# Kernel tuning notes

Measured on AMD Instinct MI355X. Metric: run time of the kernel, lower is better.

Reference implementation:

```python
import jax, jax.numpy as jnp
import numpy as np

N, DIM = 4096, 1024

def setup_inputs() -> dict:
    key = jax.random.key(0)
    ks = jax.random.split(key, 5)
    scale = 1.0 / np.sqrt(DIM)
    return {
        "x": jax.random.normal(ks[0], (N, DIM), dtype=jnp.float32),
        "Wq": jax.random.normal(ks[1], (DIM, DIM), dtype=jnp.float32) * scale,
        "bq": jax.random.normal(ks[2], (DIM,), dtype=jnp.float32) * 0.01,
        "Wk": jax.random.normal(ks[3], (DIM, DIM), dtype=jnp.float32) * scale,
        "bk": jax.random.normal(ks[4], (DIM,), dtype=jnp.float32) * 0.01,
    }

def reference(x, Wq, bq, Wk, bk):
    # torch nn.Linear: y = x @ W.T + b
    q = x @ Wq.T + bq            # [N, D]
    k = x @ Wk.T + bk            # [N, D]
    scores = q @ k.T             # [N, N] (no 1/sqrt(d) scaling, as in source)
    attn = jax.nn.softmax(scores, axis=-1)
    return attn @ x              # weighted pooling over raw x (no value proj)
```

## Files before the change

kernel.cpp:

```cpp
#include <hip/hip_runtime.h>
#include <hip/hip_bf16.h>
#include <hip/hip_fp16.h>
#include <stdint.h>


using half8   = __attribute__((ext_vector_type(8))) _Float16;
using float4v = __attribute__((ext_vector_type(4))) float;
using int4v   = __attribute__((ext_vector_type(4))) int;
using uint2v  = __attribute__((ext_vector_type(2))) unsigned int;

#define QS        (6.0f / 32768.0f)
#define INV_S     (32768.0f / 6.0f)
#define INV_S256  (128.0f / 6.0f)
#define C_HH      (65536.0f * QS * QS)
#define C_X       (256.0f * QS * QS)

#define SX        (6.0f / 32768.0f)
#define SW        (0.25f / 32768.0f)
#define P_HH      (65536.0f * SX * SW)
#define P_X       (256.0f * SX * SW)

#define GLOAD_LDS16(gptr, ldsptr)                                              \
  __builtin_amdgcn_global_load_lds(                                            \
      (__attribute__((address_space(1))) void*)(uintptr_t)(gptr),              \
      (__attribute__((address_space(3))) void*)(unsigned)(uintptr_t)(ldsptr),  \
      16, 0, 0)

__device__ __forceinline__ void barrier_raw() {
  asm volatile("" ::: "memory");
  __builtin_amdgcn_s_barrier();
  asm volatile("" ::: "memory");
}

__device__ __forceinline__ int swz3(int row) {
  return (((row >> 2) & 3) << 1) ^ (row & 3);
}

__global__ __launch_bounds__(256, 2) void gemm_s_stats(
    const int8_t* __restrict__ Ahi, const int8_t* __restrict__ Alo,
    const int8_t* __restrict__ Bhi, const int8_t* __restrict__ Blo,
    _Float16* __restrict__ E, float2* __restrict__ stats)
{
  __shared__ __align__(16) int8_t smem[65536];
  int8_t* sAh = smem;
  int8_t* sAl = smem + 16384;
  int8_t* sBh = smem + 32768;
  int8_t* sBl = smem + 49152;

  const int tid  = threadIdx.x;
  const int wave = tid >> 6;
  const int lane = tid & 63;
  const int quad = lane >> 4;
  const int t16  = lane & 15;
  const int wm   = wave & 1;
  const int wn   = wave >> 1;

  const int L    = blockIdx.y * 32 + blockIdx.x;
  const int xcd  = L & 7;
  const int idx  = L >> 3;
  const int bx   = xcd * 4 + (idx & 3);
  const int by   = idx >> 2;
  const int row0 = by * 128;
  const int col0 = bx * 128;

  const int seg  = lane & 3;
  const int rsub = lane >> 2;
  const int segS = (seg - rsub) & 3;
  const int rch  = ((quad + t16) & 3) * 16;

  const int offA0 = (row0 + wave * 16 + rsub) * 2048 + segS * 16;
  const int offA1 = offA0 + 64 * 2048;
  const int offB0 = (col0 + wave * 16 + rsub) * 2048 + segS * 16;
  const int offB1 = offB0 + 64 * 2048;
  const int ldsT0 = (wave * 16) * 64;
  const int ldsT1 = (64 + wave * 16) * 64;

  int4v hh[4][4], cc[4][4];
#pragma unroll
  for (int i = 0; i < 4; ++i)
#pragma unroll
    for (int j = 0; j < 4; ++j) {
      hh[i][j] = (int4v){0, 0, 0, 0};
      cc[i][j] = (int4v){0, 0, 0, 0};
    }

  auto stage_AhBh = [&](int ks, int b) {
    const int k0 = ks * 64;
    GLOAD_LDS16(Ahi + offA0 + k0, sAh + b * 8192 + ldsT0);
    GLOAD_LDS16(Ahi + offA1 + k0, sAh + b * 8192 + ldsT1);
    GLOAD_LDS16(Bhi + offB0 + k0, sBh + b * 8192 + ldsT0);
    GLOAD_LDS16(Bhi + offB1 + k0, sBh + b * 8192 + ldsT1);
  };
  auto stage_Bl = [&](int ks, int b) {
    const int k0 = ks * 64;
    GLOAD_LDS16(Blo + offB0 + k0, sBl + b * 8192 + ldsT0);
    GLOAD_LDS16(Blo + offB1 + k0, sBl + b * 8192 + ldsT1);
  };
  auto stage_Al = [&](int ks, int b) {
    const int k0 = ks * 64;
    GLOAD_LDS16(Alo + offA0 + k0, sAl + b * 8192 + ldsT0);
    GLOAD_LDS16(Alo + offA1 + k0, sAl + b * 8192 + ldsT1);
  };

  stage_AhBh(0, 0);
  stage_Bl(0, 0);
  stage_Al(0, 0);

  int buf = 0;
  for (int ks = 0; ks < 16; ++ks) {
    asm volatile("s_waitcnt vmcnt(4)" ::: "memory");
    barrier_raw();
    if (ks < 15) stage_AhBh(ks + 1, buf ^ 1);

    int4v ah[4], bh[4];
#pragma unroll
    for (int i = 0; i < 4; ++i)
      ah[i] = *(const int4v*)(sAh + buf * 8192 +
                              (wm * 64 + i * 16 + t16) * 64 + rch);
#pragma unroll
    for (int j = 0; j < 4; ++j)
      bh[j] = *(const int4v*)(sBh + buf * 8192 +
                              (wn * 64 + j * 16 + t16) * 64 + rch);

    __builtin_amdgcn_s_setprio(1);
#pragma unroll
    for (int i = 0; i < 4; ++i)
#pragma unroll
      for (int j = 0; j < 4; ++j)
        hh[i][j] = __builtin_amdgcn_mfma_i32_16x16x64_i8(ah[i], bh[j], hh[i][j], 0, 0, 0);
    __builtin_amdgcn_s_setprio(0);

    if (ks < 15) asm volatile("s_waitcnt vmcnt(6)" ::: "memory");
    else         asm volatile("s_waitcnt vmcnt(2)" ::: "memory");
    barrier_raw();
    if (ks < 15) stage_Bl(ks + 1, buf ^ 1);

    int4v bl[4];
#pragma unroll
    for (int j = 0; j < 4; ++j)
      bl[j] = *(const int4v*)(sBl + buf * 8192 +
                              (wn * 64 + j * 16 + t16) * 64 + rch);

    __builtin_amdgcn_s_setprio(1);
#pragma unroll
    for (int i = 0; i < 4; ++i)
#pragma unroll
      for (int j = 0; j < 4; ++j)
        cc[i][j] = __builtin_amdgcn_mfma_i32_16x16x64_i8(ah[i], bl[j], cc[i][j], 0, 0, 0);
    __builtin_amdgcn_s_setprio(0);

    if (ks < 15) asm volatile("s_waitcnt vmcnt(6)" ::: "memory");
    else         asm volatile("s_waitcnt vmcnt(0)" ::: "memory");
    barrier_raw();
    if (ks < 15) stage_Al(ks + 1, buf ^ 1);

    int4v al[4];
#pragma unroll
    for (int i = 0; i < 4; ++i)
      al[i] = *(const int4v*)(sAl + buf * 8192 +
                              (wm * 64 + i * 16 + t16) * 64 + rch);

    __builtin_amdgcn_s_setprio(1);
#pragma unroll
    for (int i = 0; i < 4; ++i)
#pragma unroll
      for (int j = 0; j < 4; ++j)
        cc[i][j] = __builtin_amdgcn_mfma_i32_16x16x64_i8(al[i], bh[j], cc[i][j], 0, 0, 0);
    __builtin_amdgcn_s_setprio(0);

    buf ^= 1;
  }

  float* red = (float*)smem;

  float vv[4][4][4];
  float rmax[4][4];
#pragma unroll
  for (int i = 0; i < 4; ++i)
#pragma unroll
    for (int r = 0; r < 4; ++r) {
      float mx = -3.0e38f;
#pragma unroll
      for (int j = 0; j < 4; ++j) {
        float v = C_HH * (float)hh[i][j][r] + C_X * (float)cc[i][j][r];
        vv[i][j][r] = v;
        mx = fmaxf(mx, v);
      }
      mx = fmaxf(mx, __shfl_xor(mx, 1));
      mx = fmaxf(mx, __shfl_xor(mx, 2));
      mx = fmaxf(mx, __shfl_xor(mx, 4));
      mx = fmaxf(mx, __shfl_xor(mx, 8));
      rmax[i][r] = mx;
    }
  if (t16 == 0) {
#pragma unroll
    for (int i = 0; i < 4; ++i)
#pragma unroll
      for (int r = 0; r < 4; ++r)
        red[wn * 128 + wm * 64 + i * 16 + quad * 4 + r] = rmax[i][r];
  }
  __syncthreads();

  float mrow[4][4];
#pragma unroll
  for (int i = 0; i < 4; ++i)
#pragma unroll
    for (int r = 0; r < 4; ++r) {
      const int row = wm * 64 + i * 16 + quad * 4 + r;
      mrow[i][r] = fmaxf(red[row], red[128 + row]);
    }

  float rsum[4][4];
#pragma unroll
  for (int i = 0; i < 4; ++i)
#pragma unroll
    for (int r = 0; r < 4; ++r) {
      float s = 0.f;
#pragma unroll
      for (int j = 0; j < 4; ++j) {
        float e = __expf(vv[i][j][r] - mrow[i][r]);
        vv[i][j][r] = e;
        s += e;
      }
      s += __shfl_xor(s, 1);
      s += __shfl_xor(s, 2);
      s += __shfl_xor(s, 4);
      s += __shfl_xor(s, 8);
      rsum[i][r] = s;
    }
  if (t16 == 0) {
#pragma unroll
    for (int i = 0; i < 4; ++i)
#pragma unroll
      for (int r = 0; r < 4; ++r)
        red[256 + wn * 128 + wm * 64 + i * 16 + quad * 4 + r] = rsum[i][r];
  }

  uint16_t* img = (uint16_t*)(smem + 32768);
#pragma unroll
  for (int i = 0; i < 4; ++i)
#pragma unroll
    for (int j = 0; j < 4; ++j)
#pragma unroll
      for (int r = 0; r < 4; ++r) {
        const int row  = wm * 64 + i * 16 + quad * 4 + r;
        const int col  = wn * 64 + j * 16 + t16;
        const int colS = col ^ (((quad << 1) ^ r) << 3);
        _Float16 h = (_Float16)vv[i][j][r];
        img[row * 128 + colS] = *(const uint16_t*)&h;
      }
  __syncthreads();

#pragma unroll
  for (int it = 0; it < 8; ++it) {
    const int row    = wave * 32 + it * 4 + quad;
    const int chunkS = t16 ^ swz3(row);
    int4v v = *(const int4v*)&img[row * 128 + chunkS * 8];
    *(int4v*)&E[(size_t)(row0 + row) * 4096 + col0 + t16 * 8] = v;
  }

  if (wn == 0 && t16 == 0) {
#pragma unroll
    for (int i = 0; i < 4; ++i)
#pragma unroll
      for (int r = 0; r < 4; ++r) {
        const int row = wm * 64 + i * 16 + quad * 4 + r;
        const float l = red[256 + row] + red[256 + 128 + row];
        stats[(size_t)(row0 + row) * 32 + bx] =
            make_float2(mrow[i][r], l);
      }
  }
}

__global__ __launch_bounds__(256, 2) void gemm_proj_i8(
    const int8_t* __restrict__ Ahi, const int8_t* __restrict__ Alo,
    const int8_t* __restrict__ Bhi, const int8_t* __restrict__ Blo,
    const float* __restrict__ biasQ, const float* __restrict__ biasK,
    int8_t* __restrict__ Ch, int8_t* __restrict__ Cl)
{
  __shared__ __align__(16) int8_t smem[65536];
  int8_t* sAh = smem;
  int8_t* sAl = smem + 16384;
  int8_t* sBh = smem + 32768;
  int8_t* sBl = smem + 49152;

  const int tid  = threadIdx.x;
  const int wave = tid >> 6;
  const int lane = tid & 63;
  const int quad = lane >> 4;
  const int t16  = lane & 15;
  const int wm   = wave & 1;
  const int wn   = wave >> 1;

  const int L    = blockIdx.y * 16 + blockIdx.x;
  const int xcd  = L & 7;
  const int idx  = L >> 3;
  const int bx   = xcd * 2 + (idx & 1);
  const int by   = idx >> 1;
  const int row0 = by * 128;
  const int col0 = bx * 128;

  const int seg  = lane & 3;
  const int rsub = lane >> 2;
  const int segS = (seg - rsub) & 3;
  const int rch  = ((quad + t16) & 3) * 16;

  const int offA0 = (row0 + wave * 16 + rsub) * 1024 + segS * 16;
  const int offA1 = offA0 + 64 * 1024;
  const int offB0 = (col0 + wave * 16 + rsub) * 1024 + segS * 16;
  const int offB1 = offB0 + 64 * 1024;
  const int ldsT0 = (wave * 16) * 64;
  const int ldsT1 = (64 + wave * 16) * 64;

  int4v hh[4][4], cc[4][4];
#pragma unroll
  for (int i = 0; i < 4; ++i)
#pragma unroll
    for (int j = 0; j < 4; ++j) {
      hh[i][j] = (int4v){0, 0, 0, 0};
      cc[i][j] = (int4v){0, 0, 0, 0};
    }

  auto stage_AhBh = [&](int ks, int b) {
    const int k0 = ks * 64;
    GLOAD_LDS16(Ahi + offA0 + k0, sAh + b * 8192 + ldsT0);
    GLOAD_LDS16(Ahi + offA1 + k0, sAh + b * 8192 + ldsT1);
    GLOAD_LDS16(Bhi + offB0 + k0, sBh + b * 8192 + ldsT0);
    GLOAD_LDS16(Bhi + offB1 + k0, sBh + b * 8192 + ldsT1);
  };
  auto stage_Bl = [&](int ks, int b) {
    const int k0 = ks * 64;
    GLOAD_LDS16(Blo + offB0 + k0, sBl + b * 8192 + ldsT0);
    GLOAD_LDS16(Blo + offB1 + k0, sBl + b * 8192 + ldsT1);
  };
  auto stage_Al = [&](int ks, int b) {
    const int k0 = ks * 64;
    GLOAD_LDS16(Alo + offA0 + k0, sAl + b * 8192 + ldsT0);
    GLOAD_LDS16(Alo + offA1 + k0, sAl + b * 8192 + ldsT1);
  };

  stage_AhBh(0, 0);
  stage_Bl(0, 0);
  stage_Al(0, 0);

  int buf = 0;
  for (int ks = 0; ks < 16; ++ks) {
    asm volatile("s_waitcnt vmcnt(4)" ::: "memory");
    barrier_raw();
    if (ks < 15) stage_AhBh(ks + 1, buf ^ 1);

    int4v ah[4], bh[4];
#pragma unroll
    for (int i = 0; i < 4; ++i)
      ah[i] = *(const int4v*)(sAh + buf * 8192 +
                              (wm * 64 + i * 16 + t16) * 64 + rch);
#pragma unroll
    for (int j = 0; j < 4; ++j)
      bh[j] = *(const int4v*)(sBh + buf * 8192 +
                              (wn * 64 + j * 16 + t16) * 64 + rch);

    __builtin_amdgcn_s_setprio(1);
#pragma unroll
    for (int i = 0; i < 4; ++i)
#pragma unroll
      for (int j = 0; j < 4; ++j)
        hh[i][j] = __builtin_amdgcn_mfma_i32_16x16x64_i8(ah[i], bh[j], hh[i][j], 0, 0, 0);
    __builtin_amdgcn_s_setprio(0);

    if (ks < 15) asm volatile("s_waitcnt vmcnt(6)" ::: "memory");
    else         asm volatile("s_waitcnt vmcnt(2)" ::: "memory");
    barrier_raw();
    if (ks < 15) stage_Bl(ks + 1, buf ^ 1);

    int4v bl[4];
#pragma unroll
    for (int j = 0; j < 4; ++j)
      bl[j] = *(const int4v*)(sBl + buf * 8192 +
                              (wn * 64 + j * 16 + t16) * 64 + rch);

    __builtin_amdgcn_s_setprio(1);
#pragma unroll
    for (int i = 0; i < 4; ++i)
#pragma unroll
      for (int j = 0; j < 4; ++j)
        cc[i][j] = __builtin_amdgcn_mfma_i32_16x16x64_i8(ah[i], bl[j], cc[i][j], 0, 0, 0);
    __builtin_amdgcn_s_setprio(0);

    if (ks < 15) asm volatile("s_waitcnt vmcnt(6)" ::: "memory");
    else         asm volatile("s_waitcnt vmcnt(0)" ::: "memory");
    barrier_raw();
    if (ks < 15) stage_Al(ks + 1, buf ^ 1);

    int4v al[4];
#pragma unroll
    for (int i = 0; i < 4; ++i)
      al[i] = *(const int4v*)(sAl + buf * 8192 +
                              (wm * 64 + i * 16 + t16) * 64 + rch);

    __builtin_amdgcn_s_setprio(1);
#pragma unroll
    for (int i = 0; i < 4; ++i)
#pragma unroll
      for (int j = 0; j < 4; ++j)
        cc[i][j] = __builtin_amdgcn_mfma_i32_16x16x64_i8(al[i], bh[j], cc[i][j], 0, 0, 0);
    __builtin_amdgcn_s_setprio(0);

    buf ^= 1;
  }

  uint16_t* img = (uint16_t*)(smem + 32768);
#pragma unroll
  for (int i = 0; i < 4; ++i) {
#pragma unroll
    for (int j = 0; j < 4; ++j) {
      const int ccol = col0 + wn * 64 + j * 16 + t16;
      const float* bp = (ccol < 1024) ? biasQ : (biasK - 1024);
#pragma unroll
      for (int r = 0; r < 4; ++r) {
        float v = P_HH * (float)hh[i][j][r] + P_X * (float)cc[i][j][r] + bp[ccol];
        int hi = (int)lrintf(v * INV_S256);
        hi = hi > 127 ? 127 : (hi < -127 ? -127 : hi);
        int lo = (int)lrintf(v * INV_S - 256.0f * (float)hi);
        lo = lo > 127 ? 127 : (lo < -127 ? -127 : lo);
        const int row  = wm * 64 + i * 16 + quad * 4 + r;
        const int col  = wn * 64 + j * 16 + t16;
        const int colS = col ^ (((quad << 1) ^ r) << 3);
        img[row * 128 + colS] = (uint16_t)((hi & 0xff) | ((lo & 0xff) << 8));
      }
    }
  }
  __syncthreads();

#pragma unroll
  for (int it = 0; it < 8; ++it) {
    const int row    = wave * 32 + it * 4 + quad;
    const int chunkS = t16 ^ swz3(row);
    int4v p = *(const int4v*)&img[row * 128 + chunkS * 8];
    const unsigned w0 = (unsigned)p[0], w1 = (unsigned)p[1];
    const unsigned w2 = (unsigned)p[2], w3 = (unsigned)p[3];
    uint2v hw, lw;
    hw[0] = (w0 & 0xffu) | (((w0 >> 16) & 0xffu) << 8) |
            ((w1 & 0xffu) << 16) | (((w1 >> 16) & 0xffu) << 24);
    hw[1] = (w2 & 0xffu) | (((w2 >> 16) & 0xffu) << 8) |
            ((w3 & 0xffu) << 16) | (((w3 >> 16) & 0xffu) << 24);
    lw[0] = ((w0 >> 8) & 0xffu) | (((w0 >> 24) & 0xffu) << 8) |
            (((w1 >> 8) & 0xffu) << 16) | ((w1 >> 24) << 24);
    lw[1] = ((w2 >> 8) & 0xffu) | (((w2 >> 24) & 0xffu) << 8) |
            (((w3 >> 8) & 0xffu) << 16) | ((w3 >> 24) << 24);
    const size_t go = (size_t)(row0 + row) * 2048 + col0 + t16 * 8;
    *(uint2v*)&Ch[go] = hw;
    *(uint2v*)&Cl[go] = lw;
  }
}

__global__ __launch_bounds__(256, 2) void gemm_av(
    const uint16_t* __restrict__ E, const uint16_t* __restrict__ B,
    const float2* __restrict__ stats, float* __restrict__ out)
{
  __shared__ __align__(16) uint16_t stg[2][12288];
  __shared__ _Float16 betaS[128 * 33];

  const int L      = blockIdx.x;
  const int xcd    = L & 7;
  const int rest   = L >> 3;
  const int colb   = rest & 15;
  const int bandHi = rest >> 4;
  const int band   = xcd + 8 * bandHi;
  const int row0   = band * 128;
  const int col0   = colb * 64;

  const int tid  = threadIdx.x;
  const int wave = tid >> 6;
  const int lane = tid & 63;
  const int quad = lane >> 4;
  const int t16  = lane & 15;
  const int wm   = wave & 1;
  const int wn   = wave >> 1;

  const int r8   = lane >> 3;
  const int c8   = lane & 7;
  const int srcC = (c8 - r8) & 7;

  int offA[4], offBx[2];
#pragma unroll
  for (int p = 0; p < 4; ++p)
    offA[p] = (row0 + p * 32 + wave * 8 + r8) * 4096 + srcC * 8;
#pragma unroll
  for (int p = 0; p < 2; ++p)
    offBx[p] = (col0 + p * 32 + wave * 8 + r8) * 4096 + srcC * 8;

  auto stage_s = [&](int s, int b) {
    const int k0h = s * 64;
    uint16_t* sA = &stg[b][0];
    uint16_t* sB = &stg[b][8192];
#pragma unroll
    for (int p = 0; p < 4; ++p)
      GLOAD_LDS16(E + offA[p] + k0h, &sA[(p * 32 + wave * 8) * 64]);
#pragma unroll
    for (int p = 0; p < 2; ++p)
      GLOAD_LDS16(B + offBx[p] + k0h, &sB[(p * 32 + wave * 8) * 64]);
  };

  stage_s(0, 0);

  if (tid < 128) {
    const int row = row0 + tid;
    float2 st[32];
    float m = -3.0e38f;
#pragma unroll
    for (int t = 0; t < 32; ++t) {
      st[t] = stats[(size_t)row * 32 + t];
      m = fmaxf(m, st[t].x);
    }
    float l = 0.f;
#pragma unroll
    for (int t = 0; t < 32; ++t) l += st[t].y * __expf(st[t].x - m);
    const float inv = 1.0f / l;
#pragma unroll
    for (int t = 0; t < 32; ++t)
      betaS[tid * 33 + t] = (_Float16)(__expf(st[t].x - m) * inv);
  }
  asm volatile("s_waitcnt vmcnt(0)" ::: "memory");
  __syncthreads();

  float4v acc[4][2];
#pragma unroll
  for (int i = 0; i < 4; ++i)
#pragma unroll
    for (int j = 0; j < 2; ++j)
      acc[i][j] = (float4v){0.f, 0.f, 0.f, 0.f};

  int buf = 0;
  for (int s = 0; s < 64; ++s) {
    if (s < 63) stage_s(s + 1, buf ^ 1);

    const int t = s >> 1;
    _Float16 bb[4];
#pragma unroll
    for (int i = 0; i < 4; ++i)
      bb[i] = betaS[(wm * 64 + i * 16 + t16) * 33 + t];

    const uint16_t* sA = &stg[buf][0];
    const uint16_t* sB = &stg[buf][8192];

    half8 af[2][4], bf[2][2];
#pragma unroll
    for (int ks = 0; ks < 2; ++ks) {
#pragma unroll
      for (int i = 0; i < 4; ++i) {
        const int row = wm * 64 + i * 16 + t16;
        const int ch  = (ks * 4 + quad + (t16 & 7)) & 7;
        af[ks][i] = *(const half8*)&sA[row * 64 + ch * 8];
        half8 bs;
#pragma unroll
        for (int c = 0; c < 8; ++c) bs[c] = bb[i];
        af[ks][i] = af[ks][i] * bs;
      }
#pragma unroll
      for (int j = 0; j < 2; ++j) {
        const int row = wn * 32 + j * 16 + t16;
        const int ch  = (ks * 4 + quad + (t16 & 7)) & 7;
        bf[ks][j] = *(const half8*)&sB[row * 64 + ch * 8];
      }
    }

    __builtin_amdgcn_s_setprio(1);
#pragma unroll
    for (int ks = 0; ks < 2; ++ks)
#pragma unroll
      for (int i = 0; i < 4; ++i)
#pragma unroll
        for (int j = 0; j < 2; ++j)
          acc[i][j] = __builtin_amdgcn_mfma_f32_16x16x32_f16(af[ks][i], bf[ks][j], acc[i][j], 0, 0, 0);
    __builtin_amdgcn_s_setprio(0);

    if (s < 63) asm volatile("s_waitcnt vmcnt(0)" ::: "memory");
    barrier_raw();
    buf ^= 1;
  }

  float* img = (float*)stg;
#pragma unroll
  for (int i = 0; i < 4; ++i)
#pragma unroll
    for (int j = 0; j < 2; ++j)
#pragma unroll
      for (int r = 0; r < 4; ++r) {
        const int row  = wm * 64 + i * 16 + quad * 4 + r;
        const int col  = wn * 32 + j * 16 + t16;
        const int colS = col ^ (swz3(row) << 2);
        img[row * 64 + colS] = acc[i][j][r];
      }
  __syncthreads();

#pragma unroll
  for (int it = 0; it < 8; ++it) {
    const int row    = wave * 32 + it * 4 + quad;
    const int chunkS = t16 ^ swz3(row);
    float4v v = *(const float4v*)&img[row * 64 + chunkS * 4];
    *(float4v*)&out[(size_t)(row0 + row) * 1024 + col0 + t16 * 4] = v;
  }
}

__global__ __launch_bounds__(256) void quantT(
    const float* __restrict__ x, const float* __restrict__ Wq,
    const float* __restrict__ Wk,
    int8_t* __restrict__ xhi, int8_t* __restrict__ xlo,
    int8_t* __restrict__ whi, int8_t* __restrict__ wlo,
    uint16_t* __restrict__ xT)
{
  if (blockIdx.x < 6144) {
    int i = blockIdx.x * 256 + threadIdx.x;
    const float* src; int8_t* dh; int8_t* dl; int idx; float s256, s;
    if (i < 1048576)      { src = x;  idx = i;           dh = xhi; dl = xlo;
                            s256 = INV_S256; s = INV_S; }
    else if (i < 1310720) { src = Wq; idx = i - 1048576; dh = whi; dl = wlo;
                            s256 = 512.0f; s = 131072.0f; }
    else                  { src = Wk; idx = i - 1310720; dh = whi + 1048576;
                            dl = wlo + 1048576; s256 = 512.0f; s = 131072.0f; }
    float4 v = ((const float4*)src)[idx];
    float vv[4] = {v.x, v.y, v.z, v.w};
    int hp = 0, lp = 0;
#pragma unroll
    for (int c = 0; c < 4; ++c) {
      int h = (int)lrintf(vv[c] * s256);
      h = h > 127 ? 127 : (h < -127 ? -127 : h);
      int l = (int)lrintf(vv[c] * s - 256.0f * (float)h);
      l = l > 127 ? 127 : (l < -127 ? -127 : l);
      hp |= (h & 0xff) << (8 * c);
      lp |= (l & 0xff) << (8 * c);
    }
    ((int*)dh)[idx] = hp;
    ((int*)dl)[idx] = lp;
  } else {
    __shared__ float tile[32][33];
    const int tb = blockIdx.x - 6144;
    const int bx = tb & 31;
    const int by = tb >> 5;
    const int tx = threadIdx.x & 31;
    const int ty = threadIdx.x >> 5;
#pragma unroll
    for (int p = 0; p < 4; ++p) {
      const int row = by * 32 + ty + p * 8;
      tile[ty + p * 8][tx] = x[(size_t)row * 1024 + bx * 32 + tx];
    }
    __syncthreads();
#pragma unroll
    for (int p = 0; p < 4; ++p) {
      const int oc = ty + p * 8;
      __half hv = __float2half_rn(tile[tx][oc]);
      xT[(size_t)(bx * 32 + oc) * 4096 + by * 32 + tx] = *(uint16_t*)&hv;
    }
  }
}

extern "C" void kernel_launch(void* const* d_in, const int* in_sizes, int n_in,
                              void* d_out, int out_size, void* d_ws, size_t ws_size,
                              hipStream_t stream) {
  const int N = 4096, D = 1024;
  const float* x  = (const float*)d_in[0];
  const float* Wq = (const float*)d_in[1];
  const float* bq = (const float*)d_in[2];
  const float* Wk = (const float*)d_in[3];
  const float* bk = (const float*)d_in[4];
  float* out = (float*)d_out;

  char* w = (char*)d_ws;
  const size_t MiB = 1024 * 1024;
  int8_t*    xq_hi  = (int8_t*)   (w + 0  * MiB);
  int8_t*    xq_lo  = (int8_t*)   (w + 4  * MiB);
  int8_t*    Wqk_hi = (int8_t*)   (w + 8  * MiB);
  int8_t*    Wqk_lo = (int8_t*)   (w + 10 * MiB);
  int8_t*    qk_hi  = (int8_t*)   (w + 12 * MiB);
  int8_t*    qk_lo  = (int8_t*)   (w + 20 * MiB);
  _Float16*  E      = (_Float16*) (w + 36 * MiB);
  float2*    stats  = (float2*)   (w + 68 * MiB);
  uint16_t*  xTh    = (uint16_t*) (w + 72 * MiB);

  quantT<<<10240, 256, 0, stream>>>(x, Wq, Wk, xq_hi, xq_lo, Wqk_hi, Wqk_lo,
                                    xTh);

  gemm_proj_i8<<<dim3(2048 / 128, N / 128), 256, 0, stream>>>(
      xq_hi, xq_lo, Wqk_hi, Wqk_lo, bq, bk, qk_hi, qk_lo);

  gemm_s_stats<<<dim3(N / 128, N / 128), 256, 0, stream>>>(
      qk_hi, qk_lo, qk_hi + 1024, qk_lo + 1024, E, stats);

  gemm_av<<<512, 256, 0, stream>>>((const uint16_t*)E, xTh, stats, out);

  (void)in_sizes; (void)n_in; (void)out_size; (void)ws_size;
}
```

Baseline: 214.7 us.

## Fuse all stages into one persistent cooperative kernel with grid syncs

Wraps the quantize/transpose, projection GEMM, score-plus-stats GEMM and attention-times-x GEMM into device functions. It runs them all in a single cooperative kernel of 512 resident blocks, separated by grid-wide syncs, which removes three kernel launch boundaries and their tail gaps. The projection and score tile mappings lose the previous XCD-aware block remapping, which may hurt L2 locality. The fixed block count serializes the score tiles two per block. If the cooperative launch fails, it falls back to the original four separate launches.

```diff
diff --git a/kernel.cpp b/kernel.cpp
--- a/kernel.cpp
+++ b/kernel.cpp
@@ -1,7 +1,10 @@
 #include <hip/hip_runtime.h>
 #include <hip/hip_bf16.h>
 #include <hip/hip_fp16.h>
+#include <hip/hip_cooperative_groups.h>
 #include <stdint.h>
+
+namespace cg = cooperative_groups;
 
 
 using half8   = __attribute__((ext_vector_type(8))) _Float16;
@@ -36,267 +39,77 @@
   return (((row >> 2) & 3) << 1) ^ (row & 3);
 }
 
-__global__ __launch_bounds__(256, 2) void gemm_s_stats(
-    const int8_t* __restrict__ Ahi, const int8_t* __restrict__ Alo,
-    const int8_t* __restrict__ Bhi, const int8_t* __restrict__ Blo,
-    _Float16* __restrict__ E, float2* __restrict__ stats)
-{
-  __shared__ __align__(16) int8_t smem[65536];
+
+__device__ __forceinline__ void quant_unit(
+    int u, int tid, const float* x, const float* Wq, const float* Wk,
+    int8_t* xhi, int8_t* xlo, int8_t* whi, int8_t* wlo)
+{
+  int i = u * 256 + tid;
+  const float* src; int8_t* dh; int8_t* dl; int idx; float s256, s;
+  if (i < 1048576)      { src = x;  idx = i;           dh = xhi; dl = xlo;
+                          s256 = INV_S256; s = INV_S; }
+  else if (i < 1310720) { src = Wq; idx = i - 1048576; dh = whi; dl = wlo;
+                          s256 = 512.0f; s = 131072.0f; }
+  else                  { src = Wk; idx = i - 1310720; dh = whi + 1048576;
+                          dl = wlo + 1048576; s256 = 512.0f; s = 131072.0f; }
+  float4 v = ((const float4*)src)[idx];
+  float vv[4] = {v.x, v.y, v.z, v.w};
+  int hp = 0, lp = 0;
+#pragma unroll
+  for (int c = 0; c < 4; ++c) {
+    int h = (int)lrintf(vv[c] * s256);
+    h = h > 127 ? 127 : (h < -127 ? -127 : h);
+    int l = (int)lrintf(vv[c] * s - 256.0f * (float)h);
+    l = l > 127 ? 127 : (l < -127 ? -127 : l);
+    hp |= (h & 0xff) << (8 * c);
+    lp |= (l & 0xff) << (8 * c);
+  }
+  ((int*)dh)[idx] = hp;
+  ((int*)dl)[idx] = lp;
+}
+
+__device__ __forceinline__ void transpose_unit(
+    int u, int tid, int8_t* smem, const float* x, uint16_t* xT)
+{
+  float (*tile)[33] = (float(*)[33])smem;
+  const int tb = u - 6144;
+  const int bx = tb & 31;
+  const int by = tb >> 5;
+  const int tx = tid & 31;
+  const int ty = tid >> 5;
+#pragma unroll
+  for (int p = 0; p < 4; ++p) {
+    const int row = by * 32 + ty + p * 8;
+    tile[ty + p * 8][tx] = x[(size_t)row * 1024 + bx * 32 + tx];
+  }
+  __syncthreads();
+#pragma unroll
+  for (int p = 0; p < 4; ++p) {
+    const int oc = ty + p * 8;
+    __half hv = __float2half_rn(tile[tx][oc]);
+    xT[(size_t)(bx * 32 + oc) * 4096 + by * 32 + tx] = *(uint16_t*)&hv;
+  }
+  __syncthreads();
+}
+
+__device__ __forceinline__ void proj_tile(
+    int bx, int by, int tid, int8_t* smem,
+    const int8_t* Ahi, const int8_t* Alo,
+    const int8_t* Bhi, const int8_t* Blo,
+    const float* biasQ, const float* biasK,
+    int8_t* Ch, int8_t* Cl)
+{
   int8_t* sAh = smem;
   int8_t* sAl = smem + 16384;
   int8_t* sBh = smem + 32768;
   int8_t* sBl = smem + 49152;
 
-  const int tid  = threadIdx.x;
   const int wave = tid >> 6;
   const int lane = tid & 63;
   const int quad = lane >> 4;
   const int t16  = lane & 15;
   const int wm   = wave & 1;
   const int wn   = wave >> 1;
-
-  const int L    = blockIdx.y * 32 + blockIdx.x;
-  const int xcd  = L & 7;
-  const int idx  = L >> 3;
-  const int bx   = xcd * 4 + (idx & 3);
-  const int by   = idx >> 2;
-  const int row0 = by * 128;
-  const int col0 = bx * 128;
-
-  const int seg  = lane & 3;
-  const int rsub = lane >> 2;
-  const int segS = (seg - rsub) & 3;
-  const int rch  = ((quad + t16) & 3) * 16;
-
-  const int offA0 = (row0 + wave * 16 + rsub) * 2048 + segS * 16;
-  const int offA1 = offA0 + 64 * 2048;
-  const int offB0 = (col0 + wave * 16 + rsub) * 2048 + segS * 16;
-  const int offB1 = offB0 + 64 * 2048;
-  const int ldsT0 = (wave * 16) * 64;
-  const int ldsT1 = (64 + wave * 16) * 64;
-
-  int4v hh[4][4], cc[4][4];
-#pragma unroll
-  for (int i = 0; i < 4; ++i)
-#pragma unroll
-    for (int j = 0; j < 4; ++j) {
-      hh[i][j] = (int4v){0, 0, 0, 0};
-      cc[i][j] = (int4v){0, 0, 0, 0};
-    }
-
-  auto stage_AhBh = [&](int ks, int b) {
-    const int k0 = ks * 64;
-    GLOAD_LDS16(Ahi + offA0 + k0, sAh + b * 8192 + ldsT0);
-    GLOAD_LDS16(Ahi + offA1 + k0, sAh + b * 8192 + ldsT1);
-    GLOAD_LDS16(Bhi + offB0 + k0, sBh + b * 8192 + ldsT0);
-    GLOAD_LDS16(Bhi + offB1 + k0, sBh + b * 8192 + ldsT1);
-  };
-  auto stage_Bl = [&](int ks, int b) {
-    const int k0 = ks * 64;
-    GLOAD_LDS16(Blo + offB0 + k0, sBl + b * 8192 + ldsT0);
-    GLOAD_LDS16(Blo + offB1 + k0, sBl + b * 8192 + ldsT1);
-  };
-  auto stage_Al = [&](int ks, int b) {
-    const int k0 = ks * 64;
-    GLOAD_LDS16(Alo + offA0 + k0, sAl + b * 8192 + ldsT0);
-    GLOAD_LDS16(Alo + offA1 + k0, sAl + b * 8192 + ldsT1);
-  };
-
-  stage_AhBh(0, 0);
-  stage_Bl(0, 0);
-  stage_Al(0, 0);
-
-  int buf = 0;
-  for (int ks = 0; ks < 16; ++ks) {
-    asm volatile("s_waitcnt vmcnt(4)" ::: "memory");
-    barrier_raw();
-    if (ks < 15) stage_AhBh(ks + 1, buf ^ 1);
-
-    int4v ah[4], bh[4];
-#pragma unroll
-    for (int i = 0; i < 4; ++i)
-      ah[i] = *(const int4v*)(sAh + buf * 8192 +
-                              (wm * 64 + i * 16 + t16) * 64 + rch);
-#pragma unroll
-    for (int j = 0; j < 4; ++j)
-      bh[j] = *(const int4v*)(sBh + buf * 8192 +
-                              (wn * 64 + j * 16 + t16) * 64 + rch);
-
-    __builtin_amdgcn_s_setprio(1);
-#pragma unroll
-    for (int i = 0; i < 4; ++i)
-#pragma unroll
-      for (int j = 0; j < 4; ++j)
-        hh[i][j] = __builtin_amdgcn_mfma_i32_16x16x64_i8(ah[i], bh[j], hh[i][j], 0, 0, 0);
-    __builtin_amdgcn_s_setprio(0);
-
-    if (ks < 15) asm volatile("s_waitcnt vmcnt(6)" ::: "memory");
-    else         asm volatile("s_waitcnt vmcnt(2)" ::: "memory");
-    barrier_raw();
-    if (ks < 15) stage_Bl(ks + 1, buf ^ 1);
-
-    int4v bl[4];
-#pragma unroll
-    for (int j = 0; j < 4; ++j)
-      bl[j] = *(const int4v*)(sBl + buf * 8192 +
-                              (wn * 64 + j * 16 + t16) * 64 + rch);
-
-    __builtin_amdgcn_s_setprio(1);
-#pragma unroll
-    for (int i = 0; i < 4; ++i)
-#pragma unroll
-      for (int j = 0; j < 4; ++j)
-        cc[i][j] = __builtin_amdgcn_mfma_i32_16x16x64_i8(ah[i], bl[j], cc[i][j], 0, 0, 0);
-    __builtin_amdgcn_s_setprio(0);
-
-    if (ks < 15) asm volatile("s_waitcnt vmcnt(6)" ::: "memory");
-    else         asm volatile("s_waitcnt vmcnt(0)" ::: "memory");
-    barrier_raw();
-    if (ks < 15) stage_Al(ks + 1, buf ^ 1);
-
-    int4v al[4];
-#pragma unroll
-    for (int i = 0; i < 4; ++i)
-      al[i] = *(const int4v*)(sAl + buf * 8192 +
-                              (wm * 64 + i * 16 + t16) * 64 + rch);
-
-    __builtin_amdgcn_s_setprio(1);
-#pragma unroll
-    for (int i = 0; i < 4; ++i)
-#pragma unroll
-      for (int j = 0; j < 4; ++j)
-        cc[i][j] = __builtin_amdgcn_mfma_i32_16x16x64_i8(al[i], bh[j], cc[i][j], 0, 0, 0);
-    __builtin_amdgcn_s_setprio(0);
-
-    buf ^= 1;
-  }
-
-  float* red = (float*)smem;
-
-  float vv[4][4][4];
-  float rmax[4][4];
-#pragma unroll
-  for (int i = 0; i < 4; ++i)
-#pragma unroll
-    for (int r = 0; r < 4; ++r) {
-      float mx = -3.0e38f;
-#pragma unroll
-      for (int j = 0; j < 4; ++j) {
-        float v = C_HH * (float)hh[i][j][r] + C_X * (float)cc[i][j][r];
-        vv[i][j][r] = v;
-        mx = fmaxf(mx, v);
-      }
-      mx = fmaxf(mx, __shfl_xor(mx, 1));
-      mx = fmaxf(mx, __shfl_xor(mx, 2));
-      mx = fmaxf(mx, __shfl_xor(mx, 4));
-      mx = fmaxf(mx, __shfl_xor(mx, 8));
-      rmax[i][r] = mx;
-    }
-  if (t16 == 0) {
-#pragma unroll
-    for (int i = 0; i < 4; ++i)
-#pragma unroll
-      for (int r = 0; r < 4; ++r)
-        red[wn * 128 + wm * 64 + i * 16 + quad * 4 + r] = rmax[i][r];
-  }
-  __syncthreads();
-
-  float mrow[4][4];
-#pragma unroll
-  for (int i = 0; i < 4; ++i)
-#pragma unroll
-    for (int r = 0; r < 4; ++r) {
-      const int row = wm * 64 + i * 16 + quad * 4 + r;
-      mrow[i][r] = fmaxf(red[row], red[128 + row]);
-    }
-
-  float rsum[4][4];
-#pragma unroll
-  for (int i = 0; i < 4; ++i)
-#pragma unroll
-    for (int r = 0; r < 4; ++r) {
-      float s = 0.f;
-#pragma unroll
-      for (int j = 0; j < 4; ++j) {
-        float e = __expf(vv[i][j][r] - mrow[i][r]);
-        vv[i][j][r] = e;
-        s += e;
-      }
-      s += __shfl_xor(s, 1);
-      s += __shfl_xor(s, 2);
-      s += __shfl_xor(s, 4);
-      s += __shfl_xor(s, 8);
-      rsum[i][r] = s;
-    }
-  if (t16 == 0) {
-#pragma unroll
-    for (int i = 0; i < 4; ++i)
-#pragma unroll
-      for (int r = 0; r < 4; ++r)
-        red[256 + wn * 128 + wm * 64 + i * 16 + quad * 4 + r] = rsum[i][r];
-  }
-
-  uint16_t* img = (uint16_t*)(smem + 32768);
-#pragma unroll
-  for (int i = 0; i < 4; ++i)
-#pragma unroll
-    for (int j = 0; j < 4; ++j)
-#pragma unroll
-      for (int r = 0; r < 4; ++r) {
-        const int row  = wm * 64 + i * 16 + quad * 4 + r;
-        const int col  = wn * 64 + j * 16 + t16;
-        const int colS = col ^ (((quad << 1) ^ r) << 3);
-        _Float16 h = (_Float16)vv[i][j][r];
-        img[row * 128 + colS] = *(const uint16_t*)&h;
-      }
-  __syncthreads();
-
-#pragma unroll
-  for (int it = 0; it < 8; ++it) {
-    const int row    = wave * 32 + it * 4 + quad;
-    const int chunkS = t16 ^ swz3(row);
-    int4v v = *(const int4v*)&img[row * 128 + chunkS * 8];
-    *(int4v*)&E[(size_t)(row0 + row) * 4096 + col0 + t16 * 8] = v;
-  }
-
-  if (wn == 0 && t16 == 0) {
-#pragma unroll
-    for (int i = 0; i < 4; ++i)
-#pragma unroll
-      for (int r = 0; r < 4; ++r) {
-        const int row = wm * 64 + i * 16 + quad * 4 + r;
-        const float l = red[256 + row] + red[256 + 128 + row];
-        stats[(size_t)(row0 + row) * 32 + bx] =
-            make_float2(mrow[i][r], l);
-      }
-  }
-}
-
-__global__ __launch_bounds__(256, 2) void gemm_proj_i8(
-    const int8_t* __restrict__ Ahi, const int8_t* __restrict__ Alo,
-    const int8_t* __restrict__ Bhi, const int8_t* __restrict__ Blo,
-    const float* __restrict__ biasQ, const float* __restrict__ biasK,
-    int8_t* __restrict__ Ch, int8_t* __restrict__ Cl)
-{
-  __shared__ __align__(16) int8_t smem[65536];
-  int8_t* sAh = smem;
-  int8_t* sAl = smem + 16384;
-  int8_t* sBh = smem + 32768;
-  int8_t* sBl = smem + 49152;
-
-  const int tid  = threadIdx.x;
-  const int wave = tid >> 6;
-  const int lane = tid & 63;
-  const int quad = lane >> 4;
-  const int t16  = lane & 15;
-  const int wm   = wave & 1;
-  const int wn   = wave >> 1;
-
-  const int L    = blockIdx.y * 16 + blockIdx.x;
-  const int xcd  = L & 7;
-  const int idx  = L >> 3;
-  const int bx   = xcd * 2 + (idx & 1);
-  const int by   = idx >> 1;
   const int row0 = by * 128;
   const int col0 = bx * 128;
 
@@ -451,16 +264,247 @@
     *(uint2v*)&Ch[go] = hw;
     *(uint2v*)&Cl[go] = lw;
   }
-}
-
-__global__ __launch_bounds__(256, 2) void gemm_av(
-    const uint16_t* __restrict__ E, const uint16_t* __restrict__ B,
-    const float2* __restrict__ stats, float* __restrict__ out)
-{
-  __shared__ __align__(16) uint16_t stg[2][12288];
-  __shared__ _Float16 betaS[128 * 33];
-
-  const int L      = blockIdx.x;
+  __syncthreads();
+}
+
+__device__ __forceinline__ void sstats_tile(
+    int bx, int by, int tid, int8_t* smem,
+    const int8_t* Ahi, const int8_t* Alo,
+    const int8_t* Bhi, const int8_t* Blo,
+    _Float16* E, float2* stats)
+{
+  int8_t* sAh = smem;
+  int8_t* sAl = smem + 16384;
+  int8_t* sBh = smem + 32768;
+  int8_t* sBl = smem + 49152;
+
+  const int wave = tid >> 6;
+  const int lane = tid & 63;
+  const int quad = lane >> 4;
+  const int t16  = lane & 15;
+  const int wm   = wave & 1;
+  const int wn   = wave >> 1;
+  const int row0 = by * 128;
+  const int col0 = bx * 128;
+
+  const int seg  = lane & 3;
+  const int rsub = lane >> 2;
+  const int segS = (seg - rsub) & 3;
+  const int rch  = ((quad + t16) & 3) * 16;
+
+  const int offA0 = (row0 + wave * 16 + rsub) * 2048 + segS * 16;
+  const int offA1 = offA0 + 64 * 2048;
+  const int offB0 = (col0 + wave * 16 + rsub) * 2048 + segS * 16;
+  const int offB1 = offB0 + 64 * 2048;
+  const int ldsT0 = (wave * 16) * 64;
+  const int ldsT1 = (64 + wave * 16) * 64;
+
+  int4v hh[4][4], cc[4][4];
+#pragma unroll
+  for (int i = 0; i < 4; ++i)
+#pragma unroll
+    for (int j = 0; j < 4; ++j) {
+      hh[i][j] = (int4v){0, 0, 0, 0};
+      cc[i][j] = (int4v){0, 0, 0, 0};
+    }
+
+  auto stage_AhBh = [&](int ks, int b) {
+    const int k0 = ks * 64;
+    GLOAD_LDS16(Ahi + offA0 + k0, sAh + b * 8192 + ldsT0);
+    GLOAD_LDS16(Ahi + offA1 + k0, sAh + b * 8192 + ldsT1);
+    GLOAD_LDS16(Bhi + offB0 + k0, sBh + b * 8192 + ldsT0);
+    GLOAD_LDS16(Bhi + offB1 + k0, sBh + b * 8192 + ldsT1);
+  };
+  auto stage_Bl = [&](int ks, int b) {
+    const int k0 = ks * 64;
+    GLOAD_LDS16(Blo + offB0 + k0, sBl + b * 8192 + ldsT0);
+    GLOAD_LDS16(Blo + offB1 + k0, sBl + b * 8192 + ldsT1);
+  };
+  auto stage_Al = [&](int ks, int b) {
+    const int k0 = ks * 64;
+    GLOAD_LDS16(Alo + offA0 + k0, sAl + b * 8192 + ldsT0);
+    GLOAD_LDS16(Alo + offA1 + k0, sAl + b * 8192 + ldsT1);
+  };
+
+  stage_AhBh(0, 0);
+  stage_Bl(0, 0);
+  stage_Al(0, 0);
+
+  int buf = 0;
+  for (int ks = 0; ks < 16; ++ks) {
+    asm volatile("s_waitcnt vmcnt(4)" ::: "memory");
+    barrier_raw();
+    if (ks < 15) stage_AhBh(ks + 1, buf ^ 1);
+
+    int4v ah[4], bh[4];
+#pragma unroll
+    for (int i = 0; i < 4; ++i)
+      ah[i] = *(const int4v*)(sAh + buf * 8192 +
+                              (wm * 64 + i * 16 + t16) * 64 + rch);
+#pragma unroll
+    for (int j = 0; j < 4; ++j)
+      bh[j] = *(const int4v*)(sBh + buf * 8192 +
+                              (wn * 64 + j * 16 + t16) * 64 + rch);
+
+    __builtin_amdgcn_s_setprio(1);
+#pragma unroll
+    for (int i = 0; i < 4; ++i)
+#pragma unroll
+      for (int j = 0; j < 4; ++j)
+        hh[i][j] = __builtin_amdgcn_mfma_i32_16x16x64_i8(ah[i], bh[j], hh[i][j], 0, 0, 0);
+    __builtin_amdgcn_s_setprio(0);
+
+    if (ks < 15) asm volatile("s_waitcnt vmcnt(6)" ::: "memory");
+    else         asm volatile("s_waitcnt vmcnt(2)" ::: "memory");
+    barrier_raw();
+    if (ks < 15) stage_Bl(ks + 1, buf ^ 1);
+
+    int4v bl[4];
+#pragma unroll
+    for (int j = 0; j < 4; ++j)
+      bl[j] = *(const int4v*)(sBl + buf * 8192 +
+                              (wn * 64 + j * 16 + t16) * 64 + rch);
+
+    __builtin_amdgcn_s_setprio(1);
+#pragma unroll
+    for (int i = 0; i < 4; ++i)
+#pragma unroll
+      for (int j = 0; j < 4; ++j)
+        cc[i][j] = __builtin_amdgcn_mfma_i32_16x16x64_i8(ah[i], bl[j], cc[i][j], 0, 0, 0);
+    __builtin_amdgcn_s_setprio(0);
+
+    if (ks < 15) asm volatile("s_waitcnt vmcnt(6)" ::: "memory");
+    else         asm volatile("s_waitcnt vmcnt(0)" ::: "memory");
+    barrier_raw();
+    if (ks < 15) stage_Al(ks + 1, buf ^ 1);
+
+    int4v al[4];
+#pragma unroll
+    for (int i = 0; i < 4; ++i)
+      al[i] = *(const int4v*)(sAl + buf * 8192 +
+                              (wm * 64 + i * 16 + t16) * 64 + rch);
+
+    __builtin_amdgcn_s_setprio(1);
+#pragma unroll
+    for (int i = 0; i < 4; ++i)
+#pragma unroll
+      for (int j = 0; j < 4; ++j)
+        cc[i][j] = __builtin_amdgcn_mfma_i32_16x16x64_i8(al[i], bh[j], cc[i][j], 0, 0, 0);
+    __builtin_amdgcn_s_setprio(0);
+
+    buf ^= 1;
+  }
+
+  float* red = (float*)smem;
+
+  float vv[4][4][4];
+  float rmax[4][4];
+#pragma unroll
+  for (int i = 0; i < 4; ++i)
+#pragma unroll
+    for (int r = 0; r < 4; ++r) {
+      float mx = -3.0e38f;
+#pragma unroll
+      for (int j = 0; j < 4; ++j) {
+        float v = C_HH * (float)hh[i][j][r] + C_X * (float)cc[i][j][r];
+        vv[i][j][r] = v;
+        mx = fmaxf(mx, v);
+      }
+      mx = fmaxf(mx, __shfl_xor(mx, 1));
+      mx = fmaxf(mx, __shfl_xor(mx, 2));
+      mx = fmaxf(mx, __shfl_xor(mx, 4));
+      mx = fmaxf(mx, __shfl_xor(mx, 8));
+      rmax[i][r] = mx;
+    }
+  if (t16 == 0) {
+#pragma unroll
+    for (int i = 0; i < 4; ++i)
+#pragma unroll
+      for (int r = 0; r < 4; ++r)
+        red[wn * 128 + wm * 64 + i * 16 + quad * 4 + r] = rmax[i][r];
+  }
+  __syncthreads();
+
+  float mrow[4][4];
+#pragma unroll
+  for (int i = 0; i < 4; ++i)
+#pragma unroll
+    for (int r = 0; r < 4; ++r) {
+      const int row = wm * 64 + i * 16 + quad * 4 + r;
+      mrow[i][r] = fmaxf(red[row], red[128 + row]);
+    }
+
+  float rsum[4][4];
+#pragma unroll
+  for (int i = 0; i < 4; ++i)
+#pragma unroll
+    for (int r = 0; r < 4; ++r) {
+      float s = 0.f;
+#pragma unroll
+      for (int j = 0; j < 4; ++j) {
+        float e = __expf(vv[i][j][r] - mrow[i][r]);
+        vv[i][j][r] = e;
+        s += e;
+      }
+      s += __shfl_xor(s, 1);
+      s += __shfl_xor(s, 2);
+      s += __shfl_xor(s, 4);
+      s += __shfl_xor(s, 8);
+      rsum[i][r] = s;
+    }
+  if (t16 == 0) {
+#pragma unroll
+    for (int i = 0; i < 4; ++i)
+#pragma unroll
+      for (int r = 0; r < 4; ++r)
+        red[256 + wn * 128 + wm * 64 + i * 16 + quad * 4 + r] = rsum[i][r];
+  }
+
+  uint16_t* img = (uint16_t*)(smem + 32768);
+#pragma unroll
+  for (int i = 0; i < 4; ++i)
+#pragma unroll
+    for (int j = 0; j < 4; ++j)
+#pragma unroll
+      for (int r = 0; r < 4; ++r) {
+        const int row  = wm * 64 + i * 16 + quad * 4 + r;
+        const int col  = wn * 64 + j * 16 + t16;
+        const int colS = col ^ (((quad << 1) ^ r) << 3);
+        _Float16 h = (_Float16)vv[i][j][r];
+        img[row * 128 + colS] = *(const uint16_t*)&h;
+      }
+  __syncthreads();
+
+#pragma unroll
+  for (int it = 0; it < 8; ++it) {
+    const int row    = wave * 32 + it * 4 + quad;
+    const int chunkS = t16 ^ swz3(row);
+    int4v v = *(const int4v*)&img[row * 128 + chunkS * 8];
+    *(int4v*)&E[(size_t)(row0 + row) * 4096 + col0 + t16 * 8] = v;
+  }
+
+  if (wn == 0 && t16 == 0) {
+#pragma unroll
+    for (int i = 0; i < 4; ++i)
+#pragma unroll
+      for (int r = 0; r < 4; ++r) {
+        const int row = wm * 64 + i * 16 + quad * 4 + r;
+        const float l = red[256 + row] + red[256 + 128 + row];
+        stats[(size_t)(row0 + row) * 32 + bx] =
+            make_float2(mrow[i][r], l);
+      }
+  }
+  __syncthreads();
+}
+
+__device__ __forceinline__ void av_tile(
+    int L, int tid, int8_t* smem,
+    const uint16_t* E, const uint16_t* B,
+    const float2* stats, float* out)
+{
+  uint16_t* stg   = (uint16_t*)smem;
+  _Float16* betaS = (_Float16*)(smem + 49152);
+
   const int xcd    = L & 7;
   const int rest   = L >> 3;
   const int colb   = rest & 15;
@@ -469,7 +513,6 @@
   const int row0   = band * 128;
   const int col0   = colb * 64;
 
-  const int tid  = threadIdx.x;
   const int wave = tid >> 6;
   const int lane = tid & 63;
   const int quad = lane >> 4;
@@ -491,8 +534,8 @@
 
   auto stage_s = [&](int s, int b) {
     const int k0h = s * 64;
-    uint16_t* sA = &stg[b][0];
-    uint16_t* sB = &stg[b][8192];
+    uint16_t* sA = stg + b * 12288;
+    uint16_t* sB = stg + b * 12288 + 8192;
 #pragma unroll
     for (int p = 0; p < 4; ++p)
       GLOAD_LDS16(E + offA[p] + k0h, &sA[(p * 32 + wave * 8) * 64]);
@@ -540,8 +583,8 @@
     for (int i = 0; i < 4; ++i)
       bb[i] = betaS[(wm * 64 + i * 16 + t16) * 33 + t];
 
-    const uint16_t* sA = &stg[buf][0];
-    const uint16_t* sB = &stg[buf][8192];
+    const uint16_t* sA = stg + buf * 12288;
+    const uint16_t* sB = stg + buf * 12288 + 8192;
 
     half8 af[2][4], bf[2][2];
 #pragma unroll
@@ -602,6 +645,73 @@
   }
 }
 
+__global__ __launch_bounds__(256, 2) void fused_all(
+    const float* __restrict__ x, const float* __restrict__ Wq,
+    const float* __restrict__ Wk,
+    const float* __restrict__ bq, const float* __restrict__ bk,
+    int8_t* __restrict__ xq_hi, int8_t* __restrict__ xq_lo,
+    int8_t* __restrict__ Wqk_hi, int8_t* __restrict__ Wqk_lo,
+    int8_t* __restrict__ qk_hi, int8_t* __restrict__ qk_lo,
+    _Float16* __restrict__ E, float2* __restrict__ stats,
+    uint16_t* __restrict__ xT, float* __restrict__ out)
+{
+  __shared__ __align__(16) int8_t smem[65536];
+  cg::grid_group grid = cg::this_grid();
+  const int tid = threadIdx.x;
+  const int blk = blockIdx.x;
+
+  for (int u = blk; u < 10240; u += 512) {
+    if (u < 6144) quant_unit(u, tid, x, Wq, Wk, xq_hi, xq_lo, Wqk_hi, Wqk_lo);
+    else          transpose_unit(u, tid, smem, x, xT);
+  }
+  __threadfence();
+  grid.sync();
+
+  proj_tile(blk & 15, blk >> 4, tid, smem,
+            xq_hi, xq_lo, Wqk_hi, Wqk_lo, bq, bk, qk_hi, qk_lo);
+  __threadfence();
+  grid.sync();
+
+  for (int rep = 0; rep < 2; ++rep) {
+    const int vL = rep * 512 + blk;
+    sstats_tile(vL & 31, vL >> 5, tid, smem,
+                qk_hi, qk_lo, qk_hi + 1024, qk_lo + 1024, E, stats);
+  }
+  __threadfence();
+  grid.sync();
+
+  av_tile(blk, tid, smem, (const uint16_t*)E, xT, stats, out);
+}
+
+__global__ __launch_bounds__(256, 2) void gemm_s_stats(
+    const int8_t* __restrict__ Ahi, const int8_t* __restrict__ Alo,
+    const int8_t* __restrict__ Bhi, const int8_t* __restrict__ Blo,
+    _Float16* __restrict__ E, float2* __restrict__ stats)
+{
+  __shared__ __align__(16) int8_t smem[65536];
+  sstats_tile(blockIdx.x, blockIdx.y, threadIdx.x, smem,
+              Ahi, Alo, Bhi, Blo, E, stats);
+}
+
+__global__ __launch_bounds__(256, 2) void gemm_proj_i8(
+    const int8_t* __restrict__ Ahi, const int8_t* __restrict__ Alo,
+    const int8_t* __restrict__ Bhi, const int8_t* __restrict__ Blo,
+    const float* __restrict__ biasQ, const float* __restrict__ biasK,
+    int8_t* __restrict__ Ch, int8_t* __restrict__ Cl)
+{
+  __shared__ __align__(16) int8_t smem[65536];
+  proj_tile(blockIdx.x, blockIdx.y, threadIdx.x, smem,
+            Ahi, Alo, Bhi, Blo, biasQ, biasK, Ch, Cl);
+}
+
+__global__ __launch_bounds__(256, 2) void gemm_av(
+    const uint16_t* __restrict__ E, const uint16_t* __restrict__ B,
+    const float2* __restrict__ stats, float* __restrict__ out)
+{
+  __shared__ __align__(16) int8_t smem[65536];
+  av_tile(blockIdx.x, threadIdx.x, smem, E, B, stats, out);
+}
+
 __global__ __launch_bounds__(256) void quantT(
     const float* __restrict__ x, const float* __restrict__ Wq,
     const float* __restrict__ Wk,
@@ -609,55 +719,16 @@
     int8_t* __restrict__ whi, int8_t* __restrict__ wlo,
     uint16_t* __restrict__ xT)
 {
-  if (blockIdx.x < 6144) {
-    int i = blockIdx.x * 256 + threadIdx.x;
-    const float* src; int8_t* dh; int8_t* dl; int idx; float s256, s;
-    if (i < 1048576)      { src = x;  idx = i;           dh = xhi; dl = xlo;
-                            s256 = INV_S256; s = INV_S; }
-    else if (i < 1310720) { src = Wq; idx = i - 1048576; dh = whi; dl = wlo;
-                            s256 = 512.0f; s = 131072.0f; }
-    else                  { src = Wk; idx = i - 1310720; dh = whi + 1048576;
-                            dl = wlo + 1048576; s256 = 512.0f; s = 131072.0f; }
-    float4 v = ((const float4*)src)[idx];
-    float vv[4] = {v.x, v.y, v.z, v.w};
-    int hp = 0, lp = 0;
-#pragma unroll
-    for (int c = 0; c < 4; ++c) {
-      int h = (int)lrintf(vv[c] * s256);
-      h = h > 127 ? 127 : (h < -127 ? -127 : h);
-      int l = (int)lrintf(vv[c] * s - 256.0f * (float)h);
-      l = l > 127 ? 127 : (l < -127 ? -127 : l);
-      hp |= (h & 0xff) << (8 * c);
-      lp |= (l & 0xff) << (8 * c);
-    }
-    ((int*)dh)[idx] = hp;
-    ((int*)dl)[idx] = lp;
-  } else {
-    __shared__ float tile[32][33];
-    const int tb = blockIdx.x - 6144;
-    const int bx = tb & 31;
-    const int by = tb >> 5;
-    const int tx = threadIdx.x & 31;
-    const int ty = threadIdx.x >> 5;
-#pragma unroll
-    for (int p = 0; p < 4; ++p) {
-      const int row = by * 32 + ty + p * 8;
-      tile[ty + p * 8][tx] = x[(size_t)row * 1024 + bx * 32 + tx];
-    }
-    __syncthreads();
-#pragma unroll
-    for (int p = 0; p < 4; ++p) {
-      const int oc = ty + p * 8;
-      __half hv = __float2half_rn(tile[tx][oc]);
-      xT[(size_t)(bx * 32 + oc) * 4096 + by * 32 + tx] = *(uint16_t*)&hv;
-    }
-  }
+  __shared__ __align__(16) int8_t smem[8448];
+  if (blockIdx.x < 6144)
+    quant_unit(blockIdx.x, threadIdx.x, x, Wq, Wk, xhi, xlo, whi, wlo);
+  else
+    transpose_unit(blockIdx.x, threadIdx.x, smem, x, xT);
 }
 
 extern "C" void kernel_launch(void* const* d_in, const int* in_sizes, int n_in,
                               void* d_out, int out_size, void* d_ws, size_t ws_size,
                               hipStream_t stream) {
-  const int N = 4096, D = 1024;
   const float* x  = (const float*)d_in[0];
   const float* Wq = (const float*)d_in[1];
   const float* bq = (const float*)d_in[2];
@@ -677,16 +748,25 @@
   float2*    stats  = (float2*)   (w + 68 * MiB);
   uint16_t*  xTh    = (uint16_t*) (w + 72 * MiB);
 
-  quantT<<<10240, 256, 0, stream>>>(x, Wq, Wk, xq_hi, xq_lo, Wqk_hi, Wqk_lo,
-                                    xTh);
-
-  gemm_proj_i8<<<dim3(2048 / 128, N / 128), 256, 0, stream>>>(
-      xq_hi, xq_lo, Wqk_hi, Wqk_lo, bq, bk, qk_hi, qk_lo);
-
-  gemm_s_stats<<<dim3(N / 128, N / 128), 256, 0, stream>>>(
-      qk_hi, qk_lo, qk_hi + 1024, qk_lo + 1024, E, stats);
-
-  gemm_av<<<512, 256, 0, stream>>>((const uint16_t*)E, xTh, stats, out);
+  void* args[] = {
+    (void*)&x, (void*)&Wq, (void*)&Wk, (void*)&bq, (void*)&bk,
+    (void*)&xq_hi, (void*)&xq_lo, (void*)&Wqk_hi, (void*)&Wqk_lo,
+    (void*)&qk_hi, (void*)&qk_lo, (void*)&E, (void*)&stats,
+    (void*)&xTh, (void*)&out
+  };
+  hipError_t err = hipLaunchCooperativeKernel(
+      (const void*)fused_all, dim3(512), dim3(256), args, 0, stream);
+
+  if (err != hipSuccess) {
+    (void)hipGetLastError();
+    quantT<<<10240, 256, 0, stream>>>(x, Wq, Wk, xq_hi, xq_lo, Wqk_hi, Wqk_lo,
+                                      xTh);
+    gemm_proj_i8<<<dim3(16, 32), 256, 0, stream>>>(
+        xq_hi, xq_lo, Wqk_hi, Wqk_lo, bq, bk, qk_hi, qk_lo);
+    gemm_s_stats<<<dim3(32, 32), 256, 0, stream>>>(
+        qk_hi, qk_lo, qk_hi + 1024, qk_lo + 1024, E, stats);
+    gemm_av<<<512, 256, 0, stream>>>((const uint16_t*)E, xTh, stats, out);
+  }
 
   (void)in_sizes; (void)n_in; (void)out_size; (void)ws_size;
 }
```

After: 580.8 us. +170.5%, slower.
